# Optimization experiments

Hardware: AMD Instinct MI355X
Metric: run time of the kernel (lower is better)

## Reference

```python
import jax, jax.numpy as jnp
import numpy as np

B, T, IN, H, L = 8192, 200, 4, 16, 4
MLP_IN, MLP_HID, MLP_OUT = H * T, 64, IN * 7


def _lstm_layer(x, Wih, Whh, b):
    """x: [B,T,Din]; Wih: [4H,Din]; Whh: [4H,H]; b: [4H]. Returns [B,T,H].
    PyTorch gate order: i, f, g, o."""
    xg = jnp.einsum('btd,gd->btg', x, Wih) + b  # precompute input projections [B,T,4H]
    h0 = jnp.zeros((x.shape[0], H), x.dtype)
    c0 = jnp.zeros((x.shape[0], H), x.dtype)

    def step(carry, xt):
        h, c = carry
        gates = xt + h @ Whh.T  # [B,4H]
        i, f, g, o = jnp.split(gates, 4, axis=-1)
        i = jax.nn.sigmoid(i); f = jax.nn.sigmoid(f)
        g = jnp.tanh(g); o = jax.nn.sigmoid(o)
        c = f * c + i * g
        h = o * jnp.tanh(c)
        return (h, c), h

    _, hs = jax.lax.scan(step, (h0, c0), jnp.swapaxes(xg, 0, 1))  # [T,B,H]
    return jnp.swapaxes(hs, 0, 1)


def setup_inputs() -> dict:
    key = jax.random.key(0)
    ks = jax.random.split(key, 12)
    s = 1.0 / np.sqrt(H)
    u = lambda k, shp: jax.random.uniform(k, shp, jnp.float32, -s, s)
    x = jax.random.normal(ks[0], (B, T, IN), jnp.float32)
    Wih0 = u(ks[1], (4 * H, IN))            # layer 0 input weights
    Wih_rest = u(ks[2], (L - 1, 4 * H, H))  # layers 1..3
    Whh = u(ks[3], (L, 4 * H, H))
    bih = u(ks[4], (L, 4 * H))
    bhh = u(ks[5], (L, 4 * H))
    sm = 1.0 / np.sqrt(MLP_IN)
    W1 = jax.random.uniform(ks[6], (MLP_HID, MLP_IN), jnp.float32, -sm, sm)
    b1 = jax.random.uniform(ks[7], (MLP_HID,), jnp.float32, -sm, sm)
    sm2 = 1.0 / np.sqrt(MLP_HID)
    W2 = jax.random.uniform(ks[8], (MLP_OUT, MLP_HID), jnp.float32, -sm2, sm2)
    b2 = jax.random.uniform(ks[9], (MLP_OUT,), jnp.float32, -sm2, sm2)
    return {"x": x, "Wih0": Wih0, "Wih_rest": Wih_rest, "Whh": Whh,
            "bih": bih, "bhh": bhh, "W1": W1, "b1": b1, "W2": W2, "b2": b2}


def reference(x, Wih0, Wih_rest, Whh, bih, bhh, W1, b1, W2, b2):
    h = _lstm_layer(x, Wih0, Whh[0], bih[0] + bhh[0])
    for l in range(1, L):
        h = _lstm_layer(h, Wih_rest[l - 1], Whh[l], bih[l] + bhh[l])
    flat = h.reshape(-1, H * T)  # [B, 3200]
    hid = jax.nn.relu(flat @ W1.T + b1)
    return hid @ W2.T + b2  # [B, 28]
```

## Files before the change

kernel.cpp:

```cpp
#include <hip/hip_runtime.h>
#include <hip/hip_bf16.h>


typedef short  bf16x8 __attribute__((ext_vector_type(8)));
typedef float  f32x4  __attribute__((ext_vector_type(4)));
typedef unsigned int uint2v __attribute__((ext_vector_type(2)));

namespace {
constexpr int kT    = 200;
constexpr int kOut  = 28;
constexpr int kQ    = kT / 4;
constexpr int kSteps = kQ + 4;
constexpr float kNLog2e  = -1.4426950408889634f;
constexpr float kN2Log2e = -2.8853900817779268f;
constexpr int kW1Elems = 64 * 3200;
}

union FragU { bf16x8 v; unsigned u[4]; };

__device__ __forceinline__ float fast_rcp(float v){ return __builtin_amdgcn_rcpf(v); }
__device__ __forceinline__ float fast_exp2(float v){ return __builtin_amdgcn_exp2f(v); }
__device__ __forceinline__ float sig_scaled(float p){ return fast_rcp(1.0f + fast_exp2(p)); }
__device__ __forceinline__ float tanh_true(float v){
  return fmaf(fast_rcp(1.0f + fast_exp2(kN2Log2e*v)), 2.0f, -1.0f);
}

__device__ __forceinline__ void split8(const float* v, FragU& hi, FragU& lo){
#pragma unroll
  for (int r=0;r<4;++r){
    unsigned ua=__float_as_uint(v[2*r]), ub=__float_as_uint(v[2*r+1]);
    hi.u[r] = (ua>>16) | (ub & 0xffff0000u);
    float af=__uint_as_float(ua & 0xffff0000u);
    float bf=__uint_as_float(ub & 0xffff0000u);
    float al=v[2*r]-af, bl=v[2*r+1]-bf;
    lo.u[r] = (__float_as_uint(al)>>16) | (__float_as_uint(bl) & 0xffff0000u);
  }
}

__global__ __launch_bounds__(256)
void presplit_w1(const float* __restrict__ W1,
                 short* __restrict__ W1h, short* __restrict__ W1l){
  int i = blockIdx.x*256 + threadIdx.x;
  if (i < kW1Elems){
    float v = W1[i];
    unsigned u = __float_as_uint(v);
    float hif = __uint_as_float(u & 0xffff0000u);
    float lo  = v - hif;
    W1h[i] = (short)(u >> 16);
    W1l[i] = (short)(__float_as_uint(lo) >> 16);
  }
}

#define HIDX(pp,ll,ss,sa,jj) (((((pp)*4+(ll))*4+(ss))*16+(sa))*24+(jj))

template<bool PS>
__global__ __launch_bounds__(256)
void lstm_pipe(const float* __restrict__ x,
               const float* __restrict__ Wih0,
               const float* __restrict__ Wihr,
               const float* __restrict__ Whh,
               const float* __restrict__ bih,
               const float* __restrict__ bhh,
               const float* __restrict__ W1,
               const float* __restrict__ b1,
               const float* __restrict__ W2,
               const float* __restrict__ b2,
               const short* __restrict__ W1h,
               const short* __restrict__ W1l,
               float* __restrict__ out)
{
  __shared__ unsigned short Hh[2][4][4][16][24];
  __shared__ unsigned short Hl[2][4][4][16][24];
  __shared__ float ldsR[16][68];

  const int tid  = threadIdx.x;
  const int lane = tid & 63;
  const int wv   = tid >> 6;
  const int s    = lane & 15;
  const int q    = lane >> 4;
  const int l    = wv;
  const int lm1  = (l==0) ? 0 : (l-1);
  const int sbase = blockIdx.x * 16;

  for (int i = tid; i < 2*4*4*16*24/2; i += 256){
    ((unsigned*)Hh)[i] = 0u;
    ((unsigned*)Hl)[i] = 0u;
  }

  FragU A[4][2];
#pragma unroll
  for (int tile=0;tile<4;++tile){
    const int grow = tile*16 + s;
    const float kE = (tile==2)? kN2Log2e : kNLog2e;
    float v[8];
    if (l==0){
#pragma unroll
      for (int e=0;e<8;++e){
        float w = 0.f;
        if (q==0 && e<4) w = Wih0[grow*4+e];
        if (q>=2)        w = Whh[grow*16 + (q&1)*8 + e];
        v[e] = w*kE;
      }
    } else {
#pragma unroll
      for (int e=0;e<8;++e){
        float w = (q<2) ? Wihr[((l-1)*64+grow)*16 + q*8 + e]
                        : Whh [(( l )*64+grow)*16 + (q&1)*8 + e];
        v[e] = w*kE;
      }
    }
    split8(v, A[tile][0], A[tile][1]);
  }

  f32x4 biasf[4];
#pragma unroll
  for (int tile=0;tile<4;++tile){
    const float kE = (tile==2)? kN2Log2e : kNLog2e;
#pragma unroll
    for (int r=0;r<4;++r){
      const int row = l*64 + tile*16 + 4*q + r;
      biasf[tile][r] = (bih[row] + bhh[row]) * kE;
    }
  }

  float cst[4] = {0.f,0.f,0.f,0.f};
  f32x4 mlpacc = (f32x4){0.f,0.f,0.f,0.f};

  const float* xp = x + (size_t)(sbase+s)*(kT*4);
  float4 xc0,xc1,xc2,xc3;
  if (l==0){
    xc0 = *(const float4*)(xp+ 0); xc1 = *(const float4*)(xp+ 4);
    xc2 = *(const float4*)(xp+ 8); xc3 = *(const float4*)(xp+12);
  }

  const int rowW1 = wv*16 + s;
  const short* w1hp = W1h + (size_t)rowW1*3200;
  const short* w1lp = W1l + (size_t)rowW1*3200;
  const float* w1fp = W1  + (size_t)rowW1*3200;
  FragU  pWhC0,pWlC0,pWhC1,pWlC1, pWhN0,pWlN0,pWhN1,pWlN1;
  float4 pWaC0,pWbC0,pWaC1,pWbC1, pWaN0,pWbN0,pWaN1,pWbN1;

  __syncthreads();

#pragma unroll 2
  for (int n=0; n<kSteps; ++n){
    const int p = n & 1;

    {
      const int mp = n - 3;
      if (mp >= 0 && mp < kQ){
        const int off = 64*mp + q*8;
        if (PS){
          pWhN0.v = *(const bf16x8*)(w1hp + off);
          pWlN0.v = *(const bf16x8*)(w1lp + off);
          pWhN1.v = *(const bf16x8*)(w1hp + off + 32);
          pWlN1.v = *(const bf16x8*)(w1lp + off + 32);
        } else {
          pWaN0 = *(const float4*)(w1fp + off);
          pWbN0 = *(const float4*)(w1fp + off + 4);
          pWaN1 = *(const float4*)(w1fp + off + 32);
          pWbN1 = *(const float4*)(w1fp + off + 36);
        }
      }
    }
    const int pr = n - l;
    float4 xn0,xn1,xn2,xn3;
    if (l==0 && pr+1 < kQ){
      const float* xq = xp + 16*(pr+1);
      xn0 = *(const float4*)(xq+ 0); xn1 = *(const float4*)(xq+ 4);
      xn2 = *(const float4*)(xq+ 8); xn3 = *(const float4*)(xq+12);
    }

    if (pr >= 0 && pr < kQ){
#pragma unroll
      for (int st=0; st<4; ++st){
        int rp, rl, rs;
        if (q < 2){ rp = p^1; rl = lm1; rs = st; }
        else if (st == 0){ rp = p^1; rl = l; rs = 3; }
        else { rp = p; rl = l; rs = st-1; }
        const int ridx = HIDX(rp, rl, rs, s, (q&1)*8);
        FragU Bh, Bl;
        Bh.v = *(const bf16x8*)&((const unsigned short*)Hh)[ridx];
        Bl.v = *(const bf16x8*)&((const unsigned short*)Hl)[ridx];
        if (l==0){
          const float4 xv = (st==0)?xc0:(st==1)?xc1:(st==2)?xc2:xc3;
          if (q==0){
            const unsigned u0=__float_as_uint(xv.x), u1=__float_as_uint(xv.y);
            const unsigned u2=__float_as_uint(xv.z), u3=__float_as_uint(xv.w);
            Bh.u[0] = (u0>>16)|(u1&0xffff0000u);
            Bh.u[1] = (u2>>16)|(u3&0xffff0000u);
            Bh.u[2] = 0u; Bh.u[3] = 0u;
            const float f0 = xv.x-__uint_as_float(u0&0xffff0000u);
            const float f1 = xv.y-__uint_as_float(u1&0xffff0000u);
            const float f2 = xv.z-__uint_as_float(u2&0xffff0000u);
            const float f3 = xv.w-__uint_as_float(u3&0xffff0000u);
            Bl.u[0] = (__float_as_uint(f0)>>16)|(__float_as_uint(f1)&0xffff0000u);
            Bl.u[1] = (__float_as_uint(f2)>>16)|(__float_as_uint(f3)&0xffff0000u);
            Bl.u[2] = 0u; Bl.u[3] = 0u;
          } else if (q==1){
#pragma unroll
            for (int r=0;r<4;++r){ Bh.u[r]=0u; Bl.u[r]=0u; }
          }
        }

        float si[4], sf[4], sg[4], so[4];
#pragma unroll
        for (int tile=0;tile<4;++tile){
          f32x4 acc = biasf[tile];
          acc = __builtin_amdgcn_mfma_f32_16x16x32_bf16(A[tile][0].v,Bh.v,acc,0,0,0);
          acc = __builtin_amdgcn_mfma_f32_16x16x32_bf16(A[tile][0].v,Bl.v,acc,0,0,0);
          acc = __builtin_amdgcn_mfma_f32_16x16x32_bf16(A[tile][1].v,Bh.v,acc,0,0,0);
#pragma unroll
          for (int r=0;r<4;++r){
            const float a = sig_scaled(acc[r]);
            if      (tile==0) si[r]=a;
            else if (tile==1) sf[r]=a;
            else if (tile==2) sg[r]=fmaf(a,2.f,-1.f);
            else              so[r]=a;
          }
        }
        float hn[4];
#pragma unroll
        for (int r=0;r<4;++r){
          cst[r] = fmaf(sf[r], cst[r], si[r]*sg[r]);
          hn[r] = so[r]*tanh_true(cst[r]);
        }
        {
          const unsigned u0=__float_as_uint(hn[0]), u1=__float_as_uint(hn[1]);
          const unsigned u2=__float_as_uint(hn[2]), u3=__float_as_uint(hn[3]);
          const unsigned hi01 = (u0>>16)|(u1&0xffff0000u);
          const unsigned hi23 = (u2>>16)|(u3&0xffff0000u);
          const float f0 = hn[0]-__uint_as_float(u0&0xffff0000u);
          const float f1 = hn[1]-__uint_as_float(u1&0xffff0000u);
          const float f2 = hn[2]-__uint_as_float(u2&0xffff0000u);
          const float f3 = hn[3]-__uint_as_float(u3&0xffff0000u);
          const unsigned lo01 = (__float_as_uint(f0)>>16)|(__float_as_uint(f1)&0xffff0000u);
          const unsigned lo23 = (__float_as_uint(f2)>>16)|(__float_as_uint(f3)&0xffff0000u);
          const int widx = HIDX(p, l, st, s, 4*q);
          *(uint2v*)&((unsigned short*)Hh)[widx] = (uint2v){hi01,hi23};
          *(uint2v*)&((unsigned short*)Hl)[widx] = (uint2v){lo01,lo23};
        }
      }
    }
    if (l==0 && pr+1 < kQ){ xc0=xn0; xc1=xn1; xc2=xn2; xc3=xn3; }

    {
      const int m = n - 4;
      if (m >= 0 && m < kQ){
#pragma unroll
        for (int pp=0; pp<2; ++pp){
          const int bidx = HIDX(p^1, 3, 2*pp + (q>>1), s, (q&1)*8);
          FragU Bh, Bl;
          Bh.v = *(const bf16x8*)&((const unsigned short*)Hh)[bidx];
          Bl.v = *(const bf16x8*)&((const unsigned short*)Hl)[bidx];
          FragU Ah, Al;
          if (PS){
            Ah = pp ? pWhC1 : pWhC0;
            Al = pp ? pWlC1 : pWlC0;
          } else {
            const float4 wa = pp ? pWaC1 : pWaC0;
            const float4 wb = pp ? pWbC1 : pWbC0;
            float v[8] = {wa.x,wa.y,wa.z,wa.w,wb.x,wb.y,wb.z,wb.w};
            split8(v,Ah,Al);
          }
          mlpacc = __builtin_amdgcn_mfma_f32_16x16x32_bf16(Ah.v,Bh.v,mlpacc,0,0,0);
          mlpacc = __builtin_amdgcn_mfma_f32_16x16x32_bf16(Ah.v,Bl.v,mlpacc,0,0,0);
          mlpacc = __builtin_amdgcn_mfma_f32_16x16x32_bf16(Al.v,Bh.v,mlpacc,0,0,0);
        }
      }
    }
    if (PS){ pWhC0=pWhN0; pWlC0=pWlN0; pWhC1=pWhN1; pWlC1=pWlN1; }
    else   { pWaC0=pWaN0; pWbC0=pWbN0; pWaC1=pWaN1; pWbC1=pWbN1; }
    __syncthreads();
  }

  {
    f32x4 rv;
#pragma unroll
    for (int r=0;r<4;++r)
      rv[r] = fmaxf(mlpacc[r] + b1[wv*16 + 4*q + r], 0.f);
    *(f32x4*)&ldsR[s][wv*16 + 4*q] = rv;
  }
  __syncthreads();
  {
    const int o  = lane & 31;
    const int oc = (o < kOut) ? o : 0;
    float4 w2r[16];
#pragma unroll
    for (int c2=0;c2<16;++c2) w2r[c2] = *(const float4*)(W2 + oc*64 + 4*c2);
    const float bias2 = b2[oc];
#pragma unroll
    for (int mm=0;mm<2;++mm){
      const int s2 = wv*4 + 2*mm + (lane>>5);
      float a0=bias2, a1=0.f, a2=0.f, a3=0.f;
#pragma unroll
      for (int c2=0;c2<16;++c2){
        const float4 rvv = *(const float4*)&ldsR[s2][4*c2];
        a0 = fmaf(w2r[c2].x, rvv.x, a0);
        a1 = fmaf(w2r[c2].y, rvv.y, a1);
        a2 = fmaf(w2r[c2].z, rvv.z, a2);
        a3 = fmaf(w2r[c2].w, rvv.w, a3);
      }
      if (o < kOut) out[(size_t)(sbase+s2)*kOut + o] = (a0+a1)+(a2+a3);
    }
  }
}

extern "C" void kernel_launch(void* const* d_in, const int* in_sizes, int n_in,
                              void* d_out, int out_size, void* d_ws, size_t ws_size,
                              hipStream_t stream) {
  (void)in_sizes; (void)n_in; (void)out_size;
  const float* x    = (const float*)d_in[0];
  const float* Wih0 = (const float*)d_in[1];
  const float* Wihr = (const float*)d_in[2];
  const float* Whh  = (const float*)d_in[3];
  const float* bih  = (const float*)d_in[4];
  const float* bhh  = (const float*)d_in[5];
  const float* W1   = (const float*)d_in[6];
  const float* b1   = (const float*)d_in[7];
  const float* W2   = (const float*)d_in[8];
  const float* b2   = (const float*)d_in[9];
  float* out = (float*)d_out;

  const size_t splitBytes = (size_t)kW1Elems * sizeof(short) * 2;
  dim3 grid(8192/16), block(256);
  if (ws_size >= splitBytes) {
    short* W1h = (short*)d_ws;
    short* W1l = W1h + kW1Elems;
    hipLaunchKernelGGL(presplit_w1, dim3((kW1Elems+255)/256), dim3(256), 0, stream,
                       W1, W1h, W1l);
    hipLaunchKernelGGL(lstm_pipe<true>, grid, block, 0, stream,
                       x, Wih0, Wihr, Whh, bih, bhh, W1, b1, W2, b2, W1h, W1l, out);
  } else {
    hipLaunchKernelGGL(lstm_pipe<false>, grid, block, 0, stream,
                       x, Wih0, Wihr, Whh, bih, bhh, W1, b1, W2, b2,
                       (const short*)nullptr, (const short*)nullptr, out);
  }
}
```

Baseline: 265.5 us.

## Interleave hi/lo bf16 state in padded LDS rows with precomputed per-parity pointers

Merges the separate hi and lo LDS state arrays into one buffer where each sample row holds hi and lo halves side by side. Rows are padded to 40 shorts. The loop is manually unrolled by parity, and per-lane read and write pointers are precomputed so the HIDX index arithmetic disappears from the inner step. The W1 prefetch, which used to be issued a step ahead in rotating registers, is now loaded inside the same step it is consumed. This cuts address computation and may change LDS bank conflicts, but it exposes global load latency before the MLP MFMAs.

```diff
diff --git a/kernel.cpp b/kernel.cpp
--- a/kernel.cpp
+++ b/kernel.cpp
@@ -14,6 +14,10 @@
 constexpr float kNLog2e  = -1.4426950408889634f;
 constexpr float kN2Log2e = -2.8853900817779268f;
 constexpr int kW1Elems = 64 * 3200;
+constexpr int kRow  = 40;
+constexpr int kSlot = 16 * kRow;
+constexpr int kLay  = 4 * kSlot;
+constexpr int kPar  = 4 * kLay;
 }
 
 union FragU { bf16x8 v; unsigned u[4]; };
@@ -50,8 +54,6 @@
     W1l[i] = (short)(__float_as_uint(lo) >> 16);
   }
 }
-
-#define HIDX(pp,ll,ss,sa,jj) (((((pp)*4+(ll))*4+(ss))*16+(sa))*24+(jj))
 
 template<bool PS>
 __global__ __launch_bounds__(256)
@@ -69,8 +71,7 @@
                const short* __restrict__ W1l,
                float* __restrict__ out)
 {
-  __shared__ unsigned short Hh[2][4][4][16][24];
-  __shared__ unsigned short Hl[2][4][4][16][24];
+  __shared__ unsigned short H[2*kPar];
   __shared__ float ldsR[16][68];
 
   const int tid  = threadIdx.x;
@@ -82,10 +83,7 @@
   const int lm1  = (l==0) ? 0 : (l-1);
   const int sbase = blockIdx.x * 16;
 
-  for (int i = tid; i < 2*4*4*16*24/2; i += 256){
-    ((unsigned*)Hh)[i] = 0u;
-    ((unsigned*)Hl)[i] = 0u;
-  }
+  for (int i = tid; i < 2*kPar/2; i += 256) ((unsigned*)H)[i] = 0u;
 
   FragU A[4][2];
 #pragma unroll
@@ -137,30 +135,38 @@
   const short* w1hp = W1h + (size_t)rowW1*3200;
   const short* w1lp = W1l + (size_t)rowW1*3200;
   const float* w1fp = W1  + (size_t)rowW1*3200;
-  FragU  pWhC0,pWlC0,pWhC1,pWlC1, pWhN0,pWlN0,pWhN1,pWlN1;
-  float4 pWaC0,pWbC0,pWaC1,pWbC1, pWaN0,pWbN0,pWaN1,pWbN1;
+
+  const int laneRd = s*kRow + (q&1)*8;
+  const int laneWr = s*kRow + q*4;
+  auto OFF = [](int par,int layer,int slot){ return par*kPar + layer*kLay + slot*kSlot; };
+  const unsigned short* ra0_0 = H + laneRd + ((q<2) ? OFF(1,lm1,0) : OFF(1,l,3));
+  const unsigned short* raS_0 = H + laneRd + ((q<2) ? OFF(1,lm1,1) : OFF(0,l,0));
+  unsigned short*       wrt_0 = H + laneWr + OFF(0,l,0);
+  const unsigned short* mrd_0 = H + laneRd + OFF(1,3,0) + (q>>1)*kSlot;
+  const unsigned short* ra0_1 = H + laneRd + ((q<2) ? OFF(0,lm1,0) : OFF(0,l,3));
+  const unsigned short* raS_1 = H + laneRd + ((q<2) ? OFF(0,lm1,1) : OFF(1,l,0));
+  unsigned short*       wrt_1 = H + laneWr + OFF(1,l,0);
+  const unsigned short* mrd_1 = H + laneRd + OFF(0,3,0) + (q>>1)*kSlot;
 
   __syncthreads();
 
-#pragma unroll 2
-  for (int n=0; n<kSteps; ++n){
-    const int p = n & 1;
-
-    {
-      const int mp = n - 3;
-      if (mp >= 0 && mp < kQ){
-        const int off = 64*mp + q*8;
-        if (PS){
-          pWhN0.v = *(const bf16x8*)(w1hp + off);
-          pWlN0.v = *(const bf16x8*)(w1lp + off);
-          pWhN1.v = *(const bf16x8*)(w1hp + off + 32);
-          pWlN1.v = *(const bf16x8*)(w1lp + off + 32);
-        } else {
-          pWaN0 = *(const float4*)(w1fp + off);
-          pWbN0 = *(const float4*)(w1fp + off + 4);
-          pWaN1 = *(const float4*)(w1fp + off + 32);
-          pWbN1 = *(const float4*)(w1fp + off + 36);
-        }
+  auto super = [&](int n, const unsigned short* ra0, const unsigned short* raS,
+                   unsigned short* wa, const unsigned short* ma){
+    const int m = n - 4;
+    FragU WAh0,WAl0,WAh1,WAl1;
+    float4 wfa0,wfb0,wfa1,wfb1;
+    if (m >= 0 && m < kQ){
+      const int off = 64*m + q*8;
+      if (PS){
+        WAh0.v = *(const bf16x8*)(w1hp + off);
+        WAl0.v = *(const bf16x8*)(w1lp + off);
+        WAh1.v = *(const bf16x8*)(w1hp + off + 32);
+        WAl1.v = *(const bf16x8*)(w1lp + off + 32);
+      } else {
+        wfa0 = *(const float4*)(w1fp + off);
+        wfb0 = *(const float4*)(w1fp + off + 4);
+        wfa1 = *(const float4*)(w1fp + off + 32);
+        wfb1 = *(const float4*)(w1fp + off + 36);
       }
     }
     const int pr = n - l;
@@ -174,14 +180,10 @@
     if (pr >= 0 && pr < kQ){
 #pragma unroll
       for (int st=0; st<4; ++st){
-        int rp, rl, rs;
-        if (q < 2){ rp = p^1; rl = lm1; rs = st; }
-        else if (st == 0){ rp = p^1; rl = l; rs = 3; }
-        else { rp = p; rl = l; rs = st-1; }
-        const int ridx = HIDX(rp, rl, rs, s, (q&1)*8);
+        const unsigned short* rp_ = (st==0) ? ra0 : (raS + (st-1)*kSlot);
         FragU Bh, Bl;
-        Bh.v = *(const bf16x8*)&((const unsigned short*)Hh)[ridx];
-        Bl.v = *(const bf16x8*)&((const unsigned short*)Hl)[ridx];
+        Bh.v = *(const bf16x8*)(rp_);
+        Bl.v = *(const bf16x8*)(rp_ + 16);
         if (l==0){
           const float4 xv = (st==0)?xc0:(st==1)?xc1:(st==2)?xc2:xc3;
           if (q==0){
@@ -236,42 +238,42 @@
           const float f3 = hn[3]-__uint_as_float(u3&0xffff0000u);
           const unsigned lo01 = (__float_as_uint(f0)>>16)|(__float_as_uint(f1)&0xffff0000u);
           const unsigned lo23 = (__float_as_uint(f2)>>16)|(__float_as_uint(f3)&0xffff0000u);
-          const int widx = HIDX(p, l, st, s, 4*q);
-          *(uint2v*)&((unsigned short*)Hh)[widx] = (uint2v){hi01,hi23};
-          *(uint2v*)&((unsigned short*)Hl)[widx] = (uint2v){lo01,lo23};
+          *(uint2v*)(wa + st*kSlot)      = (uint2v){hi01,hi23};
+          *(uint2v*)(wa + st*kSlot + 16) = (uint2v){lo01,lo23};
         }
       }
     }
     if (l==0 && pr+1 < kQ){ xc0=xn0; xc1=xn1; xc2=xn2; xc3=xn3; }
 
-    {
-      const int m = n - 4;
-      if (m >= 0 && m < kQ){
-#pragma unroll
-        for (int pp=0; pp<2; ++pp){
-          const int bidx = HIDX(p^1, 3, 2*pp + (q>>1), s, (q&1)*8);
-          FragU Bh, Bl;
-          Bh.v = *(const bf16x8*)&((const unsigned short*)Hh)[bidx];
-          Bl.v = *(const bf16x8*)&((const unsigned short*)Hl)[bidx];
-          FragU Ah, Al;
-          if (PS){
-            Ah = pp ? pWhC1 : pWhC0;
-            Al = pp ? pWlC1 : pWlC0;
-          } else {
-            const float4 wa = pp ? pWaC1 : pWaC0;
-            const float4 wb = pp ? pWbC1 : pWbC0;
-            float v[8] = {wa.x,wa.y,wa.z,wa.w,wb.x,wb.y,wb.z,wb.w};
-            split8(v,Ah,Al);
-          }
-          mlpacc = __builtin_amdgcn_mfma_f32_16x16x32_bf16(Ah.v,Bh.v,mlpacc,0,0,0);
-          mlpacc = __builtin_amdgcn_mfma_f32_16x16x32_bf16(Ah.v,Bl.v,mlpacc,0,0,0);
-          mlpacc = __builtin_amdgcn_mfma_f32_16x16x32_bf16(Al.v,Bh.v,mlpacc,0,0,0);
-        }
-      }
-    }
-    if (PS){ pWhC0=pWhN0; pWlC0=pWlN0; pWhC1=pWhN1; pWlC1=pWlN1; }
-    else   { pWaC0=pWaN0; pWbC0=pWbN0; pWaC1=pWaN1; pWbC1=pWbN1; }
+    if (m >= 0 && m < kQ){
+#pragma unroll
+      for (int pp=0; pp<2; ++pp){
+        const unsigned short* bp = ma + pp*(2*kSlot);
+        FragU Bh, Bl;
+        Bh.v = *(const bf16x8*)(bp);
+        Bl.v = *(const bf16x8*)(bp + 16);
+        FragU Ah, Al;
+        if (PS){
+          Ah = pp ? WAh1 : WAh0;
+          Al = pp ? WAl1 : WAl0;
+        } else {
+          const float4 wa4 = pp ? wfa1 : wfa0;
+          const float4 wb4 = pp ? wfb1 : wfb0;
+          float v[8] = {wa4.x,wa4.y,wa4.z,wa4.w,wb4.x,wb4.y,wb4.z,wb4.w};
+          split8(v,Ah,Al);
+        }
+        mlpacc = __builtin_amdgcn_mfma_f32_16x16x32_bf16(Ah.v,Bh.v,mlpacc,0,0,0);
+        mlpacc = __builtin_amdgcn_mfma_f32_16x16x32_bf16(Ah.v,Bl.v,mlpacc,0,0,0);
+        mlpacc = __builtin_amdgcn_mfma_f32_16x16x32_bf16(Al.v,Bh.v,mlpacc,0,0,0);
+      }
+    }
     __syncthreads();
+  };
+
+#pragma unroll 1
+  for (int n2 = 0; n2 < kSteps/2; ++n2){
+    super(2*n2,   ra0_0, raS_0, wrt_0, mrd_0);
+    super(2*n2+1, ra0_1, raS_1, wrt_1, mrd_1);
   }
 
   {
```

Measured after the change: 266.1 us. No clear change (+0.2%).
